# Kernel optimization log

Measured on AMD Instinct MI355X. Metric: run time of the kernel, lower is better.

## Reference

```python
import jax, jax.numpy as jnp
import numpy as np

T = 2048          # num tokens
H_DIM = 2048      # hidden_size
NUM_HEADS = 32    # linear_num_value_heads
NUM_KV = 16       # linear_num_key_heads
DK = 128          # linear_key_head_dim
DV = 128          # linear_value_head_dim
KCONV = 4         # linear_conv_kernel_dim
KEY_DIM = NUM_KV * DK       # 2048
VAL_DIM = NUM_HEADS * DV    # 4096
CHUNK = 64


def setup_inputs() -> dict:
    key = jax.random.key(0)
    ks = jax.random.split(key, 14)
    s = 0.02
    return {
        "hidden_states": jax.random.normal(ks[0], (T, H_DIM), jnp.float32),
        "Wq": jax.random.normal(ks[1], (H_DIM, KEY_DIM), jnp.float32) * s,
        "Wk": jax.random.normal(ks[2], (H_DIM, KEY_DIM), jnp.float32) * s,
        "Wv": jax.random.normal(ks[3], (H_DIM, VAL_DIM), jnp.float32) * s,
        "Wa": jax.random.normal(ks[4], (H_DIM, NUM_HEADS), jnp.float32) * s,
        "Wb": jax.random.normal(ks[5], (H_DIM, NUM_HEADS), jnp.float32) * s,
        "Wg": jax.random.normal(ks[6], (H_DIM, VAL_DIM), jnp.float32) * s,
        "conv_q": jax.random.normal(ks[7], (KEY_DIM, KCONV), jnp.float32) * 0.3,
        "conv_k": jax.random.normal(ks[8], (KEY_DIM, KCONV), jnp.float32) * 0.3,
        "conv_v": jax.random.normal(ks[9], (VAL_DIM, KCONV), jnp.float32) * 0.3,
        "dt_bias": jax.random.normal(ks[10], (NUM_HEADS,), jnp.float32) * 0.1,
        "A_log": jnp.log(jax.random.uniform(ks[11], (NUM_HEADS,), jnp.float32, 1.0, 8.0)),
        "o_norm_weight": 1.0 + 0.1 * jax.random.normal(ks[12], (DV,), jnp.float32),
        "Wo": jax.random.normal(ks[13], (VAL_DIM, H_DIM), jnp.float32) * s,
    }


def _causal_depthwise_conv(x, w):
    # x: [T, C], w: [C, K] -> causal depthwise conv, output [T, C]
    K = w.shape[1]
    xp = jnp.pad(x, ((K - 1, 0), (0, 0)))
    out = jax.lax.conv_general_dilated(
        xp.T[None], w[:, None, :], window_strides=(1,), padding='VALID',
        dimension_numbers=('NCH', 'OIH', 'NCH'), feature_group_count=w.shape[0])
    return out[0].T


def _l2norm(x, eps=1e-6):
    return x * jax.lax.rsqrt(jnp.sum(x * x, axis=-1, keepdims=True) + eps)


def _gdn_core(q, k, v, g, beta):
    # q,k: [T,H,DK]; v: [T,H,DV]; g,beta: [T,H]. Gated delta-rule recurrence,
    # scanned in chunks (rematerialized inner scan = chunked selective scan).
    def step(S, inp):
        qt, kt, vt, gt, bt = inp
        S = S * jnp.exp(gt)[:, None, None]                  # decay state [H,DK,DV]
        kv = jnp.einsum('hk,hkv->hv', kt, S)                # read memory at k
        dv = bt[:, None] * (vt - kv)                        # delta update
        S = S + kt[:, :, None] * dv[:, None, :]             # write outer(k, dv)
        o = jnp.einsum('hk,hkv->hv', qt, S)                 # read at q
        return S, o

    def chunk_fn(S, ch):
        return jax.lax.scan(step, S, ch)

    def resh(x):
        return x.reshape(T // CHUNK, CHUNK, *x.shape[1:])

    xs = (resh(q), resh(k), resh(v), resh(g), resh(beta))
    S0 = jnp.zeros((NUM_HEADS, DK, DV), jnp.float32)
    _, o = jax.lax.scan(jax.checkpoint(chunk_fn), S0, xs)
    return o.reshape(T, NUM_HEADS, DV)


def reference(hidden_states, Wq, Wk, Wv, Wa, Wb, Wg, conv_q, conv_k, conv_v,
              dt_bias, A_log, o_norm_weight, Wo):
    h = hidden_states
    # projections
    mixed = jnp.concatenate([h @ Wq, h @ Wk, h @ Wv], axis=-1)
    # fused causal depthwise conv1d + silu over concatenated qkv
    wconv = jnp.concatenate([conv_q, conv_k, conv_v], axis=0)
    mixed = _causal_depthwise_conv(mixed, wconv)
    mixed = mixed * jax.nn.sigmoid(mixed)  # silu activation
    q, k, v = jnp.split(mixed, [KEY_DIM, 2 * KEY_DIM], axis=-1)
    q = q.reshape(T, NUM_KV, DK)
    k = k.reshape(T, NUM_KV, DK)
    v = v.reshape(T, NUM_HEADS, DV)
    ratio = NUM_HEADS // NUM_KV
    q = jnp.repeat(q, ratio, axis=1)   # GQA expand (repeat-interleave)
    k = jnp.repeat(k, ratio, axis=1)
    q = _l2norm(q)
    k = _l2norm(k)
    # fused gating: g = -exp(A_log) * softplus(a + dt_bias); beta = sigmoid(b)
    x = h @ Wa + dt_bias
    sp = jnp.where(x <= 20.0, jax.nn.softplus(x), x)  # threshold=20, beta=1
    g = -jnp.exp(A_log) * sp                          # [T, H]
    beta = jax.nn.sigmoid(h @ Wb)                     # allow_neg_eigval=False
    o = _gdn_core(q * (DK ** -0.5), k, v, g, beta)
    # gated RMSNorm (norm before gate), eps=1e-5
    gate = (h @ Wg).reshape(T, NUM_HEADS, DV)
    o = o * jax.lax.rsqrt(jnp.mean(o * o, axis=-1, keepdims=True) + 1e-5) * o_norm_weight
    o = o * (gate * jax.nn.sigmoid(gate))
    return o.reshape(T, VAL_DIM) @ Wo
```

## Files before the change

kernel.cpp:

```cpp
#include <hip/hip_runtime.h>
#include <hip/hip_bf16.h>
#include <stdint.h>
#include <stddef.h>

using bf16 = __hip_bfloat16;
typedef __attribute__((ext_vector_type(8))) short short8;
typedef __attribute__((ext_vector_type(4))) float f32x4;
typedef __attribute__((ext_vector_type(2))) float f32x2;

#define T_TOK 2048
#define HD    2048
#define NH    32
#define NKV   16
#define DKh   128
#define DVh   128

__device__ __forceinline__ void bf2f(uint32_t u, float& a, float& b) {
    union { uint32_t i; float f; } x;
    x.i = u << 16;          a = x.f;
    x.i = u & 0xffff0000u;  b = x.f;
}

__device__ __forceinline__ void gload16(const void* g, void* l) {
    __builtin_amdgcn_global_load_lds(
        (const __attribute__((address_space(1))) void*)g,
        (__attribute__((address_space(3))) void*)l, 16, 0, 0);
}

__device__ __forceinline__ void store_c(bf16* C, size_t off, float v) { C[off] = __float2bfloat16(v); }
__device__ __forceinline__ void store_c(float* C, size_t off, float v) { C[off] = v; }

template <int CTRL>
__device__ __forceinline__ float dppadd(float x) {
    int y = __builtin_amdgcn_update_dpp(0, __float_as_int(x), CTRL, 0xf, 0xf, true);
    return x + __int_as_float(y);
}
__device__ __forceinline__ float red16(float x) {
    x = dppadd<0xB1>(x);
    x = dppadd<0x4E>(x);
    x = dppadd<0x141>(x);
    x = dppadd<0x140>(x);
    return x;
}

__device__ __forceinline__ f32x2 pkfma(f32x2 a, f32x2 b, f32x2 c) {
    return __builtin_elementwise_fma(a, b, c);
}

__global__ __launch_bounds__(256) void f2b_kernel(
    const float* __restrict__ in, bf16* __restrict__ out, int n)
{
    int i = blockIdx.x * 256 + threadIdx.x;
    if (i < n) out[i] = __float2bfloat16(in[i]);
}

__global__ __launch_bounds__(256) void transpose_kernel(
    const float* __restrict__ in, bf16* __restrict__ out, int R, int C)
{
    __shared__ bf16 tile[32][33];
    int c0 = blockIdx.x * 32, r0 = blockIdx.y * 32;
    int x = threadIdx.x;
    int y = threadIdx.y;
    #pragma unroll
    for (int i = y; i < 32; i += 8)
        tile[i][x] = __float2bfloat16(in[(size_t)(r0 + i) * C + c0 + x]);
    __syncthreads();
    #pragma unroll
    for (int i = y; i < 32; i += 8)
        out[(size_t)(c0 + i) * R + r0 + x] = tile[x][i];
}

__global__ __launch_bounds__(256) void build_wab_kernel(
    const float* __restrict__ Wa, const float* __restrict__ Wb, bf16* __restrict__ out)
{
    int k = blockIdx.x * 256 + threadIdx.x;
    int n = blockIdx.y;
    float v = 0.f;
    if (n < 32)      v = Wa[(size_t)k * 32 + n];
    else if (n < 64) v = Wb[(size_t)k * 32 + (n - 32)];
    out[(size_t)n * 2048 + k] = __float2bfloat16(v);
}

template <typename OutT>
__global__ __launch_bounds__(256) void gemm_bt_kernel(
    const bf16* __restrict__ A, const bf16* __restrict__ B, OutT* __restrict__ C,
    int M, int N, int K)
{
    __shared__ short sA[128 * 64];
    __shared__ short sB[128 * 64];
    const int tid  = threadIdx.x;
    const int w    = tid >> 6;
    const int lane = tid & 63;
    const int quad = lane >> 4;
    const int r    = lane & 15;
    const int wm   = w >> 1, wn = w & 1;
    const int bm   = blockIdx.x, bn = blockIdx.y;
    const int lrow = lane >> 3;
    const int lp   = lane & 7;
    const int lc   = lp ^ lrow;

    f32x4 acc[4][4] = {};

    const int nkb = K >> 6;
    for (int kb = 0; kb < nkb; ++kb) {
        __syncthreads();
        #pragma unroll
        for (int it = 0; it < 4; ++it) {
            int grp = w * 4 + it;
            int rr  = grp * 8 + lrow;
            const bf16* ga = A + (size_t)(bm * 128 + rr) * K + kb * 64 + lc * 8;
            gload16(ga, (void*)(sA + grp * 512));
            const bf16* gb = B + (size_t)(bn * 128 + rr) * K + kb * 64 + lc * 8;
            gload16(gb, (void*)(sB + grp * 512));
        }
        __syncthreads();

        #pragma unroll
        for (int kk = 0; kk < 2; ++kk) {
            short8 av[4], bv[4];
            #pragma unroll
            for (int i = 0; i < 4; ++i) {
                int p   = (kk * 4 + quad) ^ (r & 7);
                int row = wm * 64 + i * 16 + r;
                av[i] = *(const short8*)(sA + row * 64 + p * 8);
                int rowb = wn * 64 + i * 16 + r;
                bv[i] = *(const short8*)(sB + rowb * 64 + p * 8);
            }
            #pragma unroll
            for (int i = 0; i < 4; ++i)
                #pragma unroll
                for (int j = 0; j < 4; ++j)
                    acc[i][j] = __builtin_amdgcn_mfma_f32_16x16x32_bf16(
                        av[i], bv[j], acc[i][j], 0, 0, 0);
        }
    }

    #pragma unroll
    for (int i = 0; i < 4; ++i) {
        int row0 = bm * 128 + wm * 64 + i * 16 + quad * 4;
        #pragma unroll
        for (int j = 0; j < 4; ++j) {
            int col = bn * 128 + wn * 64 + j * 16 + r;
            #pragma unroll
            for (int e = 0; e < 4; ++e)
                store_c(C, (size_t)(row0 + e) * N + col, acc[i][j][e]);
        }
    }
}

__global__ __launch_bounds__(128) void conv_qk_kernel(
    const bf16* __restrict__ mixed, const float* __restrict__ cq,
    const float* __restrict__ ck, float* __restrict__ qn, float* __restrict__ kn)
{
    int t = blockIdx.x;
    int g = blockIdx.y;
    int d = threadIdx.x;
    int isq = (g < NKV) ? 1 : 0;
    int h   = isq ? g : g - NKV;
    int cl  = h * DKh + d;
    int c   = (isq ? 0 : 2048) + cl;
    const float* cw = isq ? cq : ck;
    float acc = 0.f;
    #pragma unroll
    for (int j = 0; j < 4; ++j) {
        int ts = t - 3 + j;
        if (ts >= 0)
            acc += __bfloat162float(mixed[(size_t)ts * 8192 + c]) * cw[cl * 4 + j];
    }
    float s = acc / (1.f + __expf(-acc));
    float ss = s * s;
    #pragma unroll
    for (int m = 1; m < 64; m <<= 1) ss += __shfl_xor(ss, m, 64);
    __shared__ float part[2];
    if ((threadIdx.x & 63) == 0) part[threadIdx.x >> 6] = ss;
    __syncthreads();
    float sum = part[0] + part[1];
    float rn = rsqrtf(sum + 1e-6f);
    float outv = s * rn;
    if (isq) outv *= 0.08838834764831845f;
    (isq ? qn : kn)[(size_t)t * 2048 + cl] = outv;
}

__global__ __launch_bounds__(256) void conv_v_kernel(
    const bf16* __restrict__ mixed, const float* __restrict__ cv, bf16* __restrict__ vv)
{
    int idx = blockIdx.x * 256 + threadIdx.x;
    int t = idx >> 12, c = idx & 4095;
    float acc = 0.f;
    #pragma unroll
    for (int j = 0; j < 4; ++j) {
        int ts = t - 3 + j;
        if (ts >= 0)
            acc += __bfloat162float(mixed[(size_t)ts * 8192 + 4096 + c]) * cv[c * 4 + j];
    }
    vv[idx] = __float2bfloat16(acc / (1.f + __expf(-acc)));
}

__global__ __launch_bounds__(256) void gating_kernel(
    const float* __restrict__ ab, const float* __restrict__ dt_bias,
    const float* __restrict__ A_log, float* __restrict__ egb2)
{
    int i = blockIdx.x * 256 + threadIdx.x;
    int t = i >> 5, h = i & 31;
    float a  = ab[(size_t)t * 128 + h] + dt_bias[h];
    float sp = (a <= 20.f) ? log1pf(__expf(a)) : a;
    float gg = -__expf(A_log[h]) * sp;
    float b = ab[(size_t)t * 128 + 32 + h];
    egb2[(size_t)i * 2]     = __expf(gg);
    egb2[(size_t)i * 2 + 1] = 1.f / (1.f + __expf(-b));
}

__device__ __forceinline__ void gdn_step(
    f32x2 S[4], float4 ka, float4 kb, float4 qa, float4 qb,
    float bvc, float egt, float nbt, bf16* optr, bool writer)
{
    f32x2 k2[4] = {{ka.x, ka.y}, {ka.z, ka.w}, {kb.x, kb.y}, {kb.z, kb.w}};
    f32x2 q2[4] = {{qa.x, qa.y}, {qa.z, qa.w}, {qb.x, qb.y}, {qb.z, qb.w}};
    f32x2 p01 = pkfma(S[1], k2[1], S[0] * k2[0]);
    f32x2 p23 = pkfma(S[3], k2[3], S[2] * k2[2]);
    f32x2 ps  = p01 + p23;
    float kv  = red16(ps.x + ps.y) * egt;
    float dvv = fmaf(nbt, kv, bvc);
    f32x2 e2 = {egt, egt}, d2 = {dvv, dvv};
    #pragma unroll
    for (int j = 0; j < 4; ++j) S[j] = pkfma(k2[j], d2, S[j] * e2);
    f32x2 o01 = pkfma(S[1], q2[1], S[0] * q2[0]);
    f32x2 o23 = pkfma(S[3], q2[3], S[2] * q2[2]);
    f32x2 os  = o01 + o23;
    float op  = red16(os.x + os.y);
    if (writer) *optr = __float2bfloat16(op);
}

#define PF_DEPTH 8

__global__ __launch_bounds__(256, 1) void recur_kernel(
    const float* __restrict__ qn, const float* __restrict__ kn, const bf16* __restrict__ vv,
    const float* __restrict__ egb, bf16* __restrict__ o)
{
    int h   = blockIdx.x;
    int sp  = blockIdx.y;
    int tid = threadIdx.x;
    int dvl = tid >> 4;
    int dkg = tid & 15;
    int dv  = sp * 16 + dvl;
    int hkv = h >> 1;
    bool writer = (dkg == 0);

    const float* kp = kn + hkv * DKh + dkg * 8;
    const float* qp = qn + hkv * DKh + dkg * 8;
    const bf16*  vp = vv + h * DVh + dv;
    const float* ep = egb + h * 2;
    bf16* optr = o + h * DVh + dv;

    f32x2 S[4] = {{0.f, 0.f}, {0.f, 0.f}, {0.f, 0.f}, {0.f, 0.f}};

    float4 ka[PF_DEPTH], kb[PF_DEPTH], qa[PF_DEPTH], qb[PF_DEPTH];
    float  es[PF_DEPTH], nb[PF_DEPTH], bv[PF_DEPTH];
    #pragma unroll
    for (int s = 0; s < PF_DEPTH; ++s) {
        ka[s] = *(const float4*)(kp + (size_t)s * 2048);
        kb[s] = *(const float4*)(kp + (size_t)s * 2048 + 4);
        qa[s] = *(const float4*)(qp + (size_t)s * 2048);
        qb[s] = *(const float4*)(qp + (size_t)s * 2048 + 4);
        float2 eb = *(const float2*)(ep + (size_t)s * 64);
        float vcf = __bfloat162float(vp[(size_t)s * 4096]);
        es[s] = eb.x; nb[s] = -eb.y; bv[s] = eb.y * vcf;
    }
    const float* kl = kp + (size_t)PF_DEPTH * 2048;
    const float* ql = qp + (size_t)PF_DEPTH * 2048;
    const bf16*  vl = vp + (size_t)PF_DEPTH * 4096;
    const float* el = ep + (size_t)PF_DEPTH * 64;

    #pragma unroll 1
    for (int t = 0; t < T_TOK; t += PF_DEPTH) {
        #pragma unroll
        for (int s = 0; s < PF_DEPTH; ++s) {
            float4 kfa = ka[s], kfb = kb[s], qfa = qa[s], qfb = qb[s];
            float egt = es[s], nbt = nb[s], bvc = bv[s];
            ka[s] = *(const float4*)(kl + (size_t)s * 2048);
            kb[s] = *(const float4*)(kl + (size_t)s * 2048 + 4);
            qa[s] = *(const float4*)(ql + (size_t)s * 2048);
            qb[s] = *(const float4*)(ql + (size_t)s * 2048 + 4);
            float2 eb = *(const float2*)(el + (size_t)s * 64);
            float vcf = __bfloat162float(vl[(size_t)s * 4096]);
            es[s] = eb.x; nb[s] = -eb.y; bv[s] = eb.y * vcf;
            gdn_step(S, kfa, kfb, qfa, qfb, bvc, egt, nbt,
                     optr + (size_t)(t + s) * 4096, writer);
        }
        kl += (size_t)PF_DEPTH * 2048;
        ql += (size_t)PF_DEPTH * 2048;
        vl += (size_t)PF_DEPTH * 4096;
        el += (size_t)PF_DEPTH * 64;
    }
}

__global__ __launch_bounds__(256) void normgate_kernel(
    const bf16* __restrict__ o, const bf16* __restrict__ gate,
    const float* __restrict__ w, bf16* __restrict__ og)
{
    int grp  = blockIdx.x * 4 + (threadIdx.x >> 6);
    int lane = threadIdx.x & 63;
    int t = grp >> 5, h = grp & 31;
    size_t base = (size_t)t * 4096 + h * DVh;
    uint32_t uo = *(const uint32_t*)(o + base + lane * 2);
    float a, b; bf2f(uo, a, b);
    float ss = a * a + b * b;
    #pragma unroll
    for (int m = 1; m < 64; m <<= 1) ss += __shfl_xor(ss, m, 64);
    float rn = rsqrtf(ss * (1.f / 128.f) + 1e-5f);
    uint32_t ug = *(const uint32_t*)(gate + base + lane * 2);
    float ga, gb; bf2f(ug, ga, gb);
    float wa = w[lane * 2], wb = w[lane * 2 + 1];
    float oa = a * rn * wa * (ga / (1.f + __expf(-ga)));
    float ob = b * rn * wb * (gb / (1.f + __expf(-gb)));
    og[base + lane * 2]     = __float2bfloat16(oa);
    og[base + lane * 2 + 1] = __float2bfloat16(ob);
}

extern "C" void kernel_launch(void* const* d_in, const int* in_sizes, int n_in,
                              void* d_out, int out_size, void* d_ws, size_t ws_size,
                              hipStream_t stream)
{
    const float* h       = (const float*)d_in[0];
    const float* Wq      = (const float*)d_in[1];
    const float* Wk      = (const float*)d_in[2];
    const float* Wv      = (const float*)d_in[3];
    const float* Wa      = (const float*)d_in[4];
    const float* Wb      = (const float*)d_in[5];
    const float* Wg      = (const float*)d_in[6];
    const float* conv_q  = (const float*)d_in[7];
    const float* conv_k  = (const float*)d_in[8];
    const float* conv_v  = (const float*)d_in[9];
    const float* dt_bias = (const float*)d_in[10];
    const float* A_log   = (const float*)d_in[11];
    const float* onw     = (const float*)d_in[12];
    const float* Wo      = (const float*)d_in[13];
    float* out = (float*)d_out;

    char* ws = (char*)d_ws;
    bf16*  WqkvT = (bf16*)ws;   ws += (size_t)8192 * 2048 * 2;
    bf16*  WgT   = (bf16*)ws;   ws += (size_t)4096 * 2048 * 2;
    bf16*  WoT   = (bf16*)ws;   ws += (size_t)2048 * 4096 * 2;
    bf16*  WabT  = (bf16*)ws;   ws += (size_t)128 * 2048 * 2;
    bf16*  hb    = (bf16*)ws;   ws += (size_t)2048 * 2048 * 2;
    bf16*  mixed = (bf16*)ws;   ws += (size_t)2048 * 8192 * 2;
    float* ab    = (float*)ws;  ws += (size_t)2048 * 128 * 4;
    float* knb   = (float*)ws;  ws += (size_t)2048 * 2048 * 4;
    bf16*  vvb   = (bf16*)ws;   ws += (size_t)2048 * 4096 * 2;
    float* egb2  = (float*)ws;  ws += (size_t)2048 * 64 * 4;
    ws += 32768;
    float* qnb = (float*)WgT;
    bf16*  ob   = WqkvT;
    bf16*  gate = WqkvT + (size_t)2048 * 4096;
    bf16*  og   = mixed;

    dim3 tb(32, 8);
    transpose_kernel<<<dim3(64, 64),  tb, 0, stream>>>(Wq, WqkvT,                       2048, 2048);
    transpose_kernel<<<dim3(64, 64),  tb, 0, stream>>>(Wk, WqkvT + (size_t)2048 * 2048, 2048, 2048);
    transpose_kernel<<<dim3(128, 64), tb, 0, stream>>>(Wv, WqkvT + (size_t)4096 * 2048, 2048, 4096);
    transpose_kernel<<<dim3(128, 64), tb, 0, stream>>>(Wg, WgT,                         2048, 4096);
    transpose_kernel<<<dim3(64, 128), tb, 0, stream>>>(Wo, WoT,                         4096, 2048);
    build_wab_kernel<<<dim3(8, 128), 256, 0, stream>>>(Wa, Wb, WabT);
    f2b_kernel<<<16384, 256, 0, stream>>>(h, hb, 2048 * 2048);

    gemm_bt_kernel<bf16> <<<dim3(16, 64), 256, 0, stream>>>(hb, WqkvT, mixed, 2048, 8192, 2048);
    gemm_bt_kernel<float><<<dim3(16, 1),  256, 0, stream>>>(hb, WabT,  ab,    2048, 128,  2048);
    gemm_bt_kernel<bf16> <<<dim3(16, 32), 256, 0, stream>>>(hb, WgT,   gate,  2048, 4096, 2048);

    conv_qk_kernel<<<dim3(2048, 32), 128, 0, stream>>>(mixed, conv_q, conv_k, qnb, knb);
    conv_v_kernel<<<32768, 256, 0, stream>>>(mixed, conv_v, vvb);
    gating_kernel<<<256, 256, 0, stream>>>(ab, dt_bias, A_log, egb2);

    recur_kernel<<<dim3(32, 8), 256, 0, stream>>>(qnb, knb, vvb, egb2, ob);
    normgate_kernel<<<16384, 256, 0, stream>>>(ob, gate, onw, og);

    gemm_bt_kernel<float><<<dim3(16, 16), 256, 0, stream>>>(og, WoT, out, 2048, 2048, 4096);
}
```

Baseline: 978.4 us.

## Reformulate delta-rule step to overlap both reductions using precomputed q·k

Rewrites the gated delta-rule step so the query output is computed from the old state: o = e·(q·S) + (q·k)·dv. This lets the k·S and q·S cross-lane reductions run together instead of one after the other on the serial path. The conv kernel now processes q and k jointly and writes the per-token q·k scalar into a packed gating buffer, alongside e, -β·e and β. The cost is a larger gating buffer and slightly different floating-point rounding.

```diff
diff --git a/kernel.cpp b/kernel.cpp
--- a/kernel.cpp
+++ b/kernel.cpp
@@ -35,12 +35,11 @@
     int y = __builtin_amdgcn_update_dpp(0, __float_as_int(x), CTRL, 0xf, 0xf, true);
     return x + __int_as_float(y);
 }
-__device__ __forceinline__ float red16(float x) {
-    x = dppadd<0xB1>(x);
-    x = dppadd<0x4E>(x);
-    x = dppadd<0x141>(x);
-    x = dppadd<0x140>(x);
-    return x;
+__device__ __forceinline__ void red16x2(float& x, float& y) {
+    x = dppadd<0xB1>(x);  y = dppadd<0xB1>(y);
+    x = dppadd<0x4E>(x);  y = dppadd<0x4E>(y);
+    x = dppadd<0x141>(x); y = dppadd<0x141>(y);
+    x = dppadd<0x140>(x); y = dppadd<0x140>(y);
 }
 
 __device__ __forceinline__ f32x2 pkfma(f32x2 a, f32x2 b, f32x2 c) {
@@ -150,35 +149,50 @@
 
 __global__ __launch_bounds__(128) void conv_qk_kernel(
     const bf16* __restrict__ mixed, const float* __restrict__ cq,
-    const float* __restrict__ ck, float* __restrict__ qn, float* __restrict__ kn)
-{
-    int t = blockIdx.x;
-    int g = blockIdx.y;
-    int d = threadIdx.x;
-    int isq = (g < NKV) ? 1 : 0;
-    int h   = isq ? g : g - NKV;
-    int cl  = h * DKh + d;
-    int c   = (isq ? 0 : 2048) + cl;
-    const float* cw = isq ? cq : ck;
-    float acc = 0.f;
+    const float* __restrict__ ck, float* __restrict__ qn, float* __restrict__ kn,
+    float* __restrict__ pk4)
+{
+    int t   = blockIdx.x;
+    int hkv = blockIdx.y;
+    int d   = threadIdx.x;
+    int cl  = hkv * DKh + d;
+    float aq = 0.f, ak = 0.f;
     #pragma unroll
     for (int j = 0; j < 4; ++j) {
         int ts = t - 3 + j;
-        if (ts >= 0)
-            acc += __bfloat162float(mixed[(size_t)ts * 8192 + c]) * cw[cl * 4 + j];
-    }
-    float s = acc / (1.f + __expf(-acc));
-    float ss = s * s;
-    #pragma unroll
-    for (int m = 1; m < 64; m <<= 1) ss += __shfl_xor(ss, m, 64);
-    __shared__ float part[2];
-    if ((threadIdx.x & 63) == 0) part[threadIdx.x >> 6] = ss;
+        if (ts >= 0) {
+            aq += __bfloat162float(mixed[(size_t)ts * 8192 + cl])        * cq[cl * 4 + j];
+            ak += __bfloat162float(mixed[(size_t)ts * 8192 + 2048 + cl]) * ck[cl * 4 + j];
+        }
+    }
+    float sq = aq / (1.f + __expf(-aq));
+    float sk = ak / (1.f + __expf(-ak));
+    float s0 = sq * sq, s1 = sk * sk, s2 = sq * sk;
+    #pragma unroll
+    for (int m = 1; m < 64; m <<= 1) {
+        s0 += __shfl_xor(s0, m, 64);
+        s1 += __shfl_xor(s1, m, 64);
+        s2 += __shfl_xor(s2, m, 64);
+    }
+    __shared__ float part[6];
+    if ((threadIdx.x & 63) == 0) {
+        int w = threadIdx.x >> 6;
+        part[w * 3 + 0] = s0; part[w * 3 + 1] = s1; part[w * 3 + 2] = s2;
+    }
     __syncthreads();
-    float sum = part[0] + part[1];
-    float rn = rsqrtf(sum + 1e-6f);
-    float outv = s * rn;
-    if (isq) outv *= 0.08838834764831845f;
-    (isq ? qn : kn)[(size_t)t * 2048 + cl] = outv;
+    float sumq = part[0] + part[3];
+    float sumk = part[1] + part[4];
+    float sqk  = part[2] + part[5];
+    float rnq = rsqrtf(sumq + 1e-6f);
+    float rnk = rsqrtf(sumk + 1e-6f);
+    const float scale = 0.08838834764831845f;
+    qn[(size_t)t * 2048 + cl] = sq * rnq * scale;
+    kn[(size_t)t * 2048 + cl] = sk * rnk;
+    if (d == 0) {
+        float qk = sqk * rnq * rnk * scale;
+        pk4[((size_t)t * 32 + 2 * hkv)     * 4 + 3] = qk;
+        pk4[((size_t)t * 32 + 2 * hkv + 1) * 4 + 3] = qk;
+    }
 }
 
 __global__ __launch_bounds__(256) void conv_v_kernel(
@@ -198,44 +212,52 @@
 
 __global__ __launch_bounds__(256) void gating_kernel(
     const float* __restrict__ ab, const float* __restrict__ dt_bias,
-    const float* __restrict__ A_log, float* __restrict__ egb2)
+    const float* __restrict__ A_log, float* __restrict__ pk4)
 {
     int i = blockIdx.x * 256 + threadIdx.x;
     int t = i >> 5, h = i & 31;
     float a  = ab[(size_t)t * 128 + h] + dt_bias[h];
     float sp = (a <= 20.f) ? log1pf(__expf(a)) : a;
     float gg = -__expf(A_log[h]) * sp;
-    float b = ab[(size_t)t * 128 + 32 + h];
-    egb2[(size_t)i * 2]     = __expf(gg);
-    egb2[(size_t)i * 2 + 1] = 1.f / (1.f + __expf(-b));
+    float b  = ab[(size_t)t * 128 + 32 + h];
+    float eg = __expf(gg);
+    float be = 1.f / (1.f + __expf(-b));
+    pk4[(size_t)i * 4 + 0] = eg;
+    pk4[(size_t)i * 4 + 1] = -be * eg;
+    pk4[(size_t)i * 4 + 2] = be;
 }
 
 __device__ __forceinline__ void gdn_step(
-    f32x2 S[4], float4 ka, float4 kb, float4 qa, float4 qb,
-    float bvc, float egt, float nbt, bf16* optr, bool writer)
-{
-    f32x2 k2[4] = {{ka.x, ka.y}, {ka.z, ka.w}, {kb.x, kb.y}, {kb.z, kb.w}};
-    f32x2 q2[4] = {{qa.x, qa.y}, {qa.z, qa.w}, {qb.x, qb.y}, {qb.z, qb.w}};
-    f32x2 p01 = pkfma(S[1], k2[1], S[0] * k2[0]);
-    f32x2 p23 = pkfma(S[3], k2[3], S[2] * k2[2]);
-    f32x2 ps  = p01 + p23;
-    float kv  = red16(ps.x + ps.y) * egt;
-    float dvv = fmaf(nbt, kv, bvc);
-    f32x2 e2 = {egt, egt}, d2 = {dvv, dvv};
-    #pragma unroll
-    for (int j = 0; j < 4; ++j) S[j] = pkfma(k2[j], d2, S[j] * e2);
-    f32x2 o01 = pkfma(S[1], q2[1], S[0] * q2[0]);
-    f32x2 o23 = pkfma(S[3], q2[3], S[2] * q2[2]);
-    f32x2 os  = o01 + o23;
-    float op  = red16(os.x + os.y);
-    if (writer) *optr = __float2bfloat16(op);
+    f32x2 S[4], float4 kfa, float4 kfb, float4 qfa, float4 qfb,
+    float egt, float nbt, float bvt, float qkt, bf16* optr, bool writer)
+{
+    f32x2 k2[4] = {{kfa.x, kfa.y}, {kfa.z, kfa.w}, {kfb.x, kfb.y}, {kfb.z, kfb.w}};
+    f32x2 q2[4] = {{qfa.x, qfa.y}, {qfa.z, qfa.w}, {qfb.x, qfb.y}, {qfb.z, qfb.w}};
+    f32x2 pd = pkfma(S[1], k2[1], S[0] * k2[0]);
+    f32x2 pe = pkfma(S[3], k2[3], S[2] * k2[2]);
+    f32x2 qd = pkfma(S[1], q2[1], S[0] * q2[0]);
+    f32x2 qe = pkfma(S[3], q2[3], S[2] * q2[2]);
+    f32x2 e2 = {egt, egt};
+    f32x2 Se0 = S[0] * e2, Se1 = S[1] * e2, Se2 = S[2] * e2, Se3 = S[3] * e2;
+    f32x2 ps = pd + pe;
+    f32x2 qs = qd + qe;
+    float d1 = ps.x + ps.y;
+    float d2 = qs.x + qs.y;
+    red16x2(d1, d2);
+    float dvv = fmaf(nbt, d1, bvt);
+    f32x2 dv2 = {dvv, dvv};
+    S[0] = pkfma(k2[0], dv2, Se0);
+    S[1] = pkfma(k2[1], dv2, Se1);
+    S[2] = pkfma(k2[2], dv2, Se2);
+    S[3] = pkfma(k2[3], dv2, Se3);
+    if (writer) *optr = __float2bfloat16(fmaf(qkt, dvv, egt * d2));
 }
 
 #define PF_DEPTH 8
 
 __global__ __launch_bounds__(256, 1) void recur_kernel(
     const float* __restrict__ qn, const float* __restrict__ kn, const bf16* __restrict__ vv,
-    const float* __restrict__ egb, bf16* __restrict__ o)
+    const float* __restrict__ pk4, bf16* __restrict__ o)
 {
     int h   = blockIdx.x;
     int sp  = blockIdx.y;
@@ -249,48 +271,48 @@
     const float* kp = kn + hkv * DKh + dkg * 8;
     const float* qp = qn + hkv * DKh + dkg * 8;
     const bf16*  vp = vv + h * DVh + dv;
-    const float* ep = egb + h * 2;
+    const float* gp = pk4 + h * 4;
     bf16* optr = o + h * DVh + dv;
 
     f32x2 S[4] = {{0.f, 0.f}, {0.f, 0.f}, {0.f, 0.f}, {0.f, 0.f}};
 
     float4 ka[PF_DEPTH], kb[PF_DEPTH], qa[PF_DEPTH], qb[PF_DEPTH];
-    float  es[PF_DEPTH], nb[PF_DEPTH], bv[PF_DEPTH];
+    float  es[PF_DEPTH], ns[PF_DEPTH], qs[PF_DEPTH], bv[PF_DEPTH];
     #pragma unroll
     for (int s = 0; s < PF_DEPTH; ++s) {
         ka[s] = *(const float4*)(kp + (size_t)s * 2048);
         kb[s] = *(const float4*)(kp + (size_t)s * 2048 + 4);
         qa[s] = *(const float4*)(qp + (size_t)s * 2048);
         qb[s] = *(const float4*)(qp + (size_t)s * 2048 + 4);
-        float2 eb = *(const float2*)(ep + (size_t)s * 64);
+        float4 g4 = *(const float4*)(gp + (size_t)s * 128);
         float vcf = __bfloat162float(vp[(size_t)s * 4096]);
-        es[s] = eb.x; nb[s] = -eb.y; bv[s] = eb.y * vcf;
+        es[s] = g4.x; ns[s] = g4.y; qs[s] = g4.w; bv[s] = g4.z * vcf;
     }
     const float* kl = kp + (size_t)PF_DEPTH * 2048;
     const float* ql = qp + (size_t)PF_DEPTH * 2048;
     const bf16*  vl = vp + (size_t)PF_DEPTH * 4096;
-    const float* el = ep + (size_t)PF_DEPTH * 64;
+    const float* gl = gp + (size_t)PF_DEPTH * 128;
 
     #pragma unroll 1
     for (int t = 0; t < T_TOK; t += PF_DEPTH) {
         #pragma unroll
         for (int s = 0; s < PF_DEPTH; ++s) {
             float4 kfa = ka[s], kfb = kb[s], qfa = qa[s], qfb = qb[s];
-            float egt = es[s], nbt = nb[s], bvc = bv[s];
+            float egt = es[s], nbt = ns[s], qkt = qs[s], bvt = bv[s];
             ka[s] = *(const float4*)(kl + (size_t)s * 2048);
             kb[s] = *(const float4*)(kl + (size_t)s * 2048 + 4);
             qa[s] = *(const float4*)(ql + (size_t)s * 2048);
             qb[s] = *(const float4*)(ql + (size_t)s * 2048 + 4);
-            float2 eb = *(const float2*)(el + (size_t)s * 64);
+            float4 g4 = *(const float4*)(gl + (size_t)s * 128);
             float vcf = __bfloat162float(vl[(size_t)s * 4096]);
-            es[s] = eb.x; nb[s] = -eb.y; bv[s] = eb.y * vcf;
-            gdn_step(S, kfa, kfb, qfa, qfb, bvc, egt, nbt,
+            es[s] = g4.x; ns[s] = g4.y; qs[s] = g4.w; bv[s] = g4.z * vcf;
+            gdn_step(S, kfa, kfb, qfa, qfb, egt, nbt, bvt, qkt,
                      optr + (size_t)(t + s) * 4096, writer);
         }
         kl += (size_t)PF_DEPTH * 2048;
         ql += (size_t)PF_DEPTH * 2048;
         vl += (size_t)PF_DEPTH * 4096;
-        el += (size_t)PF_DEPTH * 64;
+        gl += (size_t)PF_DEPTH * 128;
     }
 }
 
@@ -347,7 +369,7 @@
     float* ab    = (float*)ws;  ws += (size_t)2048 * 128 * 4;
     float* knb   = (float*)ws;  ws += (size_t)2048 * 2048 * 4;
     bf16*  vvb   = (bf16*)ws;   ws += (size_t)2048 * 4096 * 2;
-    float* egb2  = (float*)ws;  ws += (size_t)2048 * 64 * 4;
+    float* pk4   = (float*)ws;  ws += (size_t)2048 * 32 * 4 * 4;
     ws += 32768;
     float* qnb = (float*)WgT;
     bf16*  ob   = WqkvT;
@@ -367,11 +389,11 @@
     gemm_bt_kernel<float><<<dim3(16, 1),  256, 0, stream>>>(hb, WabT,  ab,    2048, 128,  2048);
     gemm_bt_kernel<bf16> <<<dim3(16, 32), 256, 0, stream>>>(hb, WgT,   gate,  2048, 4096, 2048);
 
-    conv_qk_kernel<<<dim3(2048, 32), 128, 0, stream>>>(mixed, conv_q, conv_k, qnb, knb);
+    conv_qk_kernel<<<dim3(2048, 16), 128, 0, stream>>>(mixed, conv_q, conv_k, qnb, knb, pk4);
     conv_v_kernel<<<32768, 256, 0, stream>>>(mixed, conv_v, vvb);
-    gating_kernel<<<256, 256, 0, stream>>>(ab, dt_bias, A_log, egb2);
-
-    recur_kernel<<<dim3(32, 8), 256, 0, stream>>>(qnb, knb, vvb, egb2, ob);
+    gating_kernel<<<256, 256, 0, stream>>>(ab, dt_bias, A_log, pk4);
+
+    recur_kernel<<<dim3(32, 8), 256, 0, stream>>>(qnb, knb, vvb, pk4, ob);
     normgate_kernel<<<16384, 256, 0, stream>>>(ob, gate, onw, og);
 
     gemm_bt_kernel<float><<<dim3(16, 16), 256, 0, stream>>>(og, WoT, out, 2048, 2048, 4096);
```

Result: no change. 960.4 us (-1.8%).
